# Kernel tuning notes

Measured on AMD Instinct MI355X. Metric: run time of the kernel, lower is better.

Reference implementation:

```python
import jax, jax.numpy as jnp
import numpy as np


def _compute_gradient(f, src, dst, egw):
    # f: [b, c, n] node features; src/dst: [b, e] edge endpoints; egw: [b, e, d]
    # gradient at node src = sum_edges pinvdx * (f[dst] - f[src])
    fT = f.transpose(0, 2, 1)  # b, n, c
    n = fT.shape[1]
    f_dst = jnp.take_along_axis(fT, dst[..., None], axis=1)  # b, e, c
    f_src = jnp.take_along_axis(fT, src[..., None], axis=1)  # b, e, c
    msg = egw[..., :, None] * (f_dst - f_src)[..., None, :]  # b, e, d, c
    b, e, d, c = msg.shape

    def seg(m, s):
        return jax.ops.segment_sum(m.reshape(e, d * c), s, num_segments=n)

    grad = jax.vmap(seg)(msg, src)  # b, n, d*c
    return grad.transpose(0, 2, 1)  # b, d*c, n


def _forward(x, t, nodes, node_weights, edge_gradient_weights, modes, sp_L,
             fc0_w, fc0_b, Wc, Ws, W0, ws_w, ws_b, gws_w, gws_b,
             fc1_w, fc1_b, fc2_w, fc2_b, directed_edges):
    D = nodes.shape[-1]
    # Fourier bases: modes [k,d,w] scaled by sp_L [d,w]
    temp = jnp.einsum('bxd,kdw->bxkw', nodes, modes * sp_L)
    bc, bs = jnp.cos(temp), jnp.sin(temp)
    b0 = jnp.ones(temp[:, :, :1, :].shape, temp.dtype)
    nw = node_weights[:, :, None, :]
    wbc, wbs, wb0 = bc * nw, bs * nw, b0 * nw

    x_value = x[:, :, :D]
    h = jnp.concatenate([x, t], -1) @ fc0_w + fc0_b  # b, n, c
    h = h.transpose(0, 2, 1)  # b, c, n

    src = directed_edges[..., 0]
    dst = directed_edges[..., 1]
    nlayers = ws_w.shape[0]
    for i in range(nlayers):
        # spectral convolution (real Fourier transform on scattered points)
        xc = jnp.einsum('bcx,bxkw->bckw', h, wbc)
        xs = -jnp.einsum('bcx,bxkw->bckw', h, wbs)
        x0 = jnp.einsum('bcx,bxkw->bckw', h, wb0)
        fc_ = jnp.einsum('bikw,iokw->bokw', xc, Wc[i]) - jnp.einsum('bikw,iokw->bokw', xs, Ws[i])
        fs_ = jnp.einsum('bikw,iokw->bokw', xs, Wc[i]) + jnp.einsum('bikw,iokw->bokw', xc, Ws[i])
        f0_ = jnp.einsum('bikw,iokw->bokw', x0, W0[i])
        x1 = (jnp.einsum('bokw,bxkw->box', f0_, b0)
              + 2.0 * jnp.einsum('bokw,bxkw->box', fc_, bc)
              - 2.0 * jnp.einsum('bokw,bxkw->box', fs_, bs))
        # pointwise linear (Conv1d kernel size 1)
        x2 = jnp.einsum('oc,bcx->box', ws_w[i], h) + ws_b[i][None, :, None]
        # gradient operator + softsign + Conv1d
        g = _compute_gradient(h, src, dst, edge_gradient_weights)  # b, d*c, n
        g = g / (1.0 + jnp.abs(g))  # softsign
        x3 = jnp.einsum('oc,bcx->box', gws_w[i], g) + gws_b[i][None, :, None]
        h = x1 + x2 + x3
        if i != nlayers - 1:
            h = jax.nn.gelu(h, approximate=False)

    h = h.transpose(0, 2, 1)  # b, n, c
    h = jax.nn.gelu(h @ fc1_w + fc1_b, approximate=False)
    h = h @ fc2_w + fc2_b
    return x_value + t * h


def setup_inputs() -> dict:
    B, N, E = 2, 20000, 100000
    D, W, K, C, L, FC, OUT = 3, 1, 128, 128, 3, 128, 3
    key = jax.random.key(0)
    k = jax.random.split(key, 16)
    x = jax.random.normal(k[0], (B, N, D), jnp.float32)
    t = jax.random.uniform(k[1], (B, N, 1), jnp.float32)
    node_mask = jnp.ones((B, N, 1), jnp.int32)
    nodes = jax.random.uniform(k[2], (B, N, D), jnp.float32)
    node_weights = jax.random.uniform(k[3], (B, N, W), jnp.float32) / N
    directed_edges = jax.random.randint(k[4], (B, E, 2), 0, N)
    edge_gradient_weights = jax.random.normal(k[5], (B, E, D), jnp.float32)
    modes = jax.random.normal(k[6], (K, D, W), jnp.float32) * (2.0 * np.pi)
    sp_L = jnp.ones((D, W), jnp.float32)
    fc0_w = jax.random.normal(k[7], (D + 1, C), jnp.float32) * 0.1
    fc0_b = jnp.zeros((C,), jnp.float32)
    scale = 1.0 / (C * C)
    Wc = jax.random.uniform(k[8], (L, C, C, K, W), jnp.float32) * scale
    Ws = jax.random.uniform(k[9], (L, C, C, K, W), jnp.float32) * scale
    W0 = jax.random.uniform(k[10], (L, C, C, 1, W), jnp.float32) * scale
    ws_w = jax.random.normal(k[11], (L, C, C), jnp.float32) * 0.05
    ws_b = jnp.zeros((L, C), jnp.float32)
    gws_w = jax.random.normal(k[12], (L, C, D * C), jnp.float32) * 0.05
    gws_b = jnp.zeros((L, C), jnp.float32)
    fc1_w = jax.random.normal(k[13], (C, FC), jnp.float32) * 0.05
    fc1_b = jnp.zeros((FC,), jnp.float32)
    fc2_w = jax.random.normal(k[14], (FC, OUT), jnp.float32) * 0.05
    fc2_b = jnp.zeros((OUT,), jnp.float32)
    return dict(x=x, t=t, node_mask=node_mask, nodes=nodes, node_weights=node_weights,
                directed_edges=directed_edges, edge_gradient_weights=edge_gradient_weights,
                modes=modes, sp_L=sp_L, fc0_w=fc0_w, fc0_b=fc0_b, Wc=Wc, Ws=Ws, W0=W0,
                ws_w=ws_w, ws_b=ws_b, gws_w=gws_w, gws_b=gws_b,
                fc1_w=fc1_w, fc1_b=fc1_b, fc2_w=fc2_w, fc2_b=fc2_b)


def reference(x, t, node_mask, nodes, node_weights, directed_edges, edge_gradient_weights,
              modes, sp_L, fc0_w, fc0_b, Wc, Ws, W0, ws_w, ws_b, gws_w, gws_b,
              fc1_w, fc1_b, fc2_w, fc2_b):
    del node_mask  # unpacked but unused in the original forward
    return _forward(x, t, nodes, node_weights, edge_gradient_weights, modes, sp_L,
                    fc0_w, fc0_b, Wc, Ws, W0, ws_w, ws_b, gws_w, gws_b,
                    fc1_w, fc1_b, fc2_w, fc2_b, directed_edges)
```

## Files before the change

kernel.cpp:

```cpp
#include <hip/hip_runtime.h>
#include <math.h>

#define BB 2
#define NN 20000
#define EE 100000
#define DD 3
#define KK 128
#define CC 128
#define LL 3
#define FCC 128
#define GJ (DD*CC)
#define KR 768
#define NP 20096
#define NCHK 157
#define G1CH 79
#define G1N 256

typedef __attribute__((ext_vector_type(8))) short bf16x8;
typedef __attribute__((ext_vector_type(4))) float f32x4;

__device__ inline unsigned short f2bf(float f) {
  unsigned int u = __float_as_uint(f);
  u += 0x7fffu + ((u >> 16) & 1u);
  return (unsigned short)(u >> 16);
}
__device__ inline float bf2f(unsigned short u) {
  return __uint_as_float(((unsigned int)u) << 16);
}

__device__ float d_nw[BB*NN];
__device__ __align__(16) unsigned short d_stackT[(size_t)BB*NP*KR];
__device__ __align__(16) unsigned short d_bcT[(size_t)BB*KK*NP];
__device__ __align__(16) unsigned short d_bsT[(size_t)BB*KK*NP];
__device__ __align__(16) unsigned short d_hTwT[(size_t)BB*CC*NP];
__device__ __align__(16) float d_uT[(size_t)BB*NP*FCC];
__device__ __align__(16) unsigned short d_Amatb[BB*CC*KR];
__device__ __align__(16) unsigned short d_fc1wb[FCC*CC];
__device__ __align__(16) float d_part[(size_t)BB*4*G1CH*2*64*64];
__device__ float d_xc[BB*CC*KK];
__device__ float d_xs[BB*CC*KK];
__device__ float d_x0p[BB*NCHK*CC];
__device__ float d_fcp[BB*CC*8*KK];
__device__ float d_fsp[BB*CC*8*KK];
__device__ float d_bias[BB*CC];
__device__ int d_cnt[BB*NN];
__device__ int d_cursor[BB*NN];
__device__ int d_off[BB*(NN+1)];
__device__ __align__(16) float4 d_erec[(size_t)BB*EE];

__global__ __launch_bounds__(128) void k_basis(const float* __restrict__ nodes,
                                               const float* __restrict__ nodew,
                                               const float* __restrict__ modes,
                                               const float* __restrict__ spL) {
  int bn = blockIdx.x;
  int k  = threadIdx.x;
  int b = bn / NN, n = bn % NN;
  float x0 = nodes[bn*3+0], x1 = nodes[bn*3+1], x2 = nodes[bn*3+2];
  float tmp = x0*modes[k*3+0]*spL[0] + x1*modes[k*3+1]*spL[1] + x2*modes[k*3+2]*spL[2];
  float cv = cosf(tmp), sv = sinf(tmp);
  size_t row = (size_t)(b*NP + n);
  d_stackT[row*KR + k]       = f2bf(cv);
  d_stackT[row*KR + 128 + k] = f2bf(sv);
  if (k == 0) d_nw[bn] = nodew[bn];
}

__global__ __launch_bounds__(256) void k_basisT() {
  __shared__ unsigned short t1[32][136];
  __shared__ unsigned short t2[32][136];
  int blk = blockIdx.x;
  int nt = blk % 628, b = blk / 628;
  int n0 = nt*32;
  int tid = threadIdx.x;
  int kl = tid & 127, ng = tid >> 7;
  for (int nn = ng; nn < 32; nn += 2) {
    int n = n0 + nn;
    unsigned short cv = 0, sv = 0;
    if (n < NN) {
      const unsigned short* sp = d_stackT + ((size_t)(b*NP + n))*KR;
      cv = sp[kl]; sv = sp[128 + kl];
    }
    t1[nn][kl] = cv;
    t2[nn][kl] = sv;
  }
  __syncthreads();
  int nl = tid & 31, kg = tid >> 5;
  for (int k = kg; k < 128; k += 8) {
    d_bcT[((size_t)(b*KK + k))*NP + n0 + nl] = t1[nl][k];
    d_bsT[((size_t)(b*KK + k))*NP + n0 + nl] = t2[nl][k];
  }
}

__global__ __launch_bounds__(256) void k_csr_zero() {
  int tid = blockIdx.x*256 + threadIdx.x;
  if (tid < BB*NN) { d_cnt[tid] = 0; d_cursor[tid] = 0; }
}

__global__ __launch_bounds__(256) void k_csr_count(const int* __restrict__ edges) {
  int e = blockIdx.x*256 + threadIdx.x;
  if (e >= BB*EE) return;
  int b = e / EE;
  int src = edges[e*2 + 0];
  atomicAdd(&d_cnt[b*NN + src], 1);
}

__global__ __launch_bounds__(1024) void k_csr_scan() {
  int b = blockIdx.x;
  __shared__ int sdata[1024];
  __shared__ int carry_s;
  int tid = threadIdx.x;
  if (tid == 0) carry_s = 0;
  __syncthreads();
  for (int chunk = 0; chunk < 20; ++chunk) {
    int i = chunk*1024 + tid;
    int v = (i < NN) ? d_cnt[b*NN + i] : 0;
    sdata[tid] = v;
    __syncthreads();
    for (int s = 1; s < 1024; s <<= 1) {
      int tv = (tid >= s) ? sdata[tid - s] : 0;
      __syncthreads();
      sdata[tid] += tv;
      __syncthreads();
    }
    int excl = carry_s + sdata[tid] - v;
    if (i < NN) d_off[b*(NN+1) + i] = excl;
    __syncthreads();
    if (tid == 1023) carry_s += sdata[1023];
    __syncthreads();
  }
  if (tid == 0) d_off[b*(NN+1) + NN] = carry_s;
}

__global__ __launch_bounds__(256) void k_csr_scatter(const int* __restrict__ edges,
                                                     const float* __restrict__ egw) {
  int e = blockIdx.x*256 + threadIdx.x;
  if (e >= BB*EE) return;
  int b = e / EE;
  int src = edges[e*2 + 0];
  int dst = edges[e*2 + 1];
  int pos = atomicAdd(&d_cursor[b*NN + src], 1);
  d_erec[(size_t)b*EE + d_off[b*(NN+1) + src] + pos] =
      make_float4(__int_as_float(dst), egw[e*3+0], egw[e*3+1], egw[e*3+2]);
}

__global__ __launch_bounds__(256) void k_h0(const float* __restrict__ x,
                                            const float* __restrict__ t,
                                            const float* __restrict__ w,
                                            const float* __restrict__ bias) {
  int tid = blockIdx.x*256 + threadIdx.x;
  int c = tid & 127;
  int bn = tid >> 7;
  int b = bn / NN, n = bn % NN;
  const float* xv = x + bn*3;
  float acc = bias[c] + xv[0]*w[c] + xv[1]*w[CC+c] + xv[2]*w[2*CC+c]
            + t[bn]*w[3*CC+c];
  d_stackT[((size_t)(b*NP + n))*KR + 256 + c] = f2bf(acc);
}

__global__ __launch_bounds__(256) void k_hT0() {
  __shared__ unsigned short t[128][136];
  int chunk = blockIdx.x;
  int b = blockIdx.y;
  int n0 = chunk*128;
  int tid = threadIdx.x;
  int cl = tid & 127, ng = tid >> 7;
  for (int nn = ng; nn < 128; nn += 2) {
    int n = n0 + nn;
    unsigned short v = 0;
    if (n < NN) {
      float hv = bf2f(d_stackT[((size_t)(b*NP + n))*KR + 256 + cl]);
      v = f2bf(hv * d_nw[b*NN + n]);
    }
    t[nn][cl] = v;
  }
  __syncthreads();
  int nl = tid & 31, cg = tid >> 5;
  for (int c = cg; c < 128; c += 8)
    for (int nn2 = 0; nn2 < 128; nn2 += 32)
      d_hTwT[((size_t)(b*CC + c))*NP + n0 + nn2 + nl] = t[nn2 + nl][c];
}

__global__ __launch_bounds__(256) void k_gemm1m() {
  __shared__ unsigned short Ash[2][64*40];
  __shared__ unsigned short Bch[2][64*40];
  __shared__ unsigned short Bsh[2][64*40];
  int chunk = blockIdx.x;
  int quad  = blockIdx.y;
  int b     = blockIdx.z;
  int ch = quad >> 1, kh = quad & 1;
  int tid = threadIdx.x, lane = tid & 63, wid = tid >> 6;
  int q = lane >> 4, m = lane & 15;
  f32x4 accC[4], accS[4];
  #pragma unroll
  for (int j = 0; j < 4; j++) { accC[j] = (f32x4){0.f,0.f,0.f,0.f}; accS[j] = (f32x4){0.f,0.f,0.f,0.f}; }
  const unsigned short* Ab  = d_hTwT + ((size_t)(b*CC + ch*64))*NP;
  const unsigned short* Bcp = d_bcT + ((size_t)(b*KK + kh*64))*NP;
  const unsigned short* Bsp = d_bsT + ((size_t)(b*KK + kh*64))*NP;
  int n0 = chunk*G1N;

#define G1STAGE(nb, d) { \
    int row_ = tid >> 2; int e8_ = (tid & 3)*8; \
    if ((nb) < NP) { \
      *(uint4*)&Ash[d][row_*40 + e8_] = *(const uint4*)(Ab  + (size_t)row_*NP + (nb) + e8_); \
      *(uint4*)&Bch[d][row_*40 + e8_] = *(const uint4*)(Bcp + (size_t)row_*NP + (nb) + e8_); \
      *(uint4*)&Bsh[d][row_*40 + e8_] = *(const uint4*)(Bsp + (size_t)row_*NP + (nb) + e8_); \
    } else { \
      uint4 z_ = make_uint4(0,0,0,0); \
      *(uint4*)&Ash[d][row_*40 + e8_] = z_; \
      *(uint4*)&Bch[d][row_*40 + e8_] = z_; \
      *(uint4*)&Bsh[d][row_*40 + e8_] = z_; \
    } }

  G1STAGE(n0, 0)
  int cur = 0;
  for (int s = 0; s < G1N/32; s++) {
    __syncthreads();
    if (s + 1 < G1N/32) G1STAGE(n0 + (s+1)*32, cur ^ 1)
    bf16x8 a = *(const bf16x8*)&Ash[cur][(wid*16 + m)*40 + q*8];
    #pragma unroll
    for (int kt = 0; kt < 4; kt++) {
      bf16x8 bcf = *(const bf16x8*)&Bch[cur][(kt*16 + m)*40 + q*8];
      accC[kt] = __builtin_amdgcn_mfma_f32_16x16x32_bf16(a, bcf, accC[kt], 0, 0, 0);
      bf16x8 bsf = *(const bf16x8*)&Bsh[cur][(kt*16 + m)*40 + q*8];
      accS[kt] = __builtin_amdgcn_mfma_f32_16x16x32_bf16(a, bsf, accS[kt], 0, 0, 0);
    }
    cur ^= 1;
  }
#undef G1STAGE

  float* base = d_part + ((size_t)(b*4 + quad)*G1CH + chunk)*2*4096;
  #pragma unroll
  for (int kt = 0; kt < 4; kt++)
    #pragma unroll
    for (int r = 0; r < 4; r++) {
      int c = wid*16 + q*4 + r;
      int k = kt*16 + m;
      base[c*64 + k]        =  accC[kt][r];
      base[4096 + c*64 + k] = -accS[kt][r];
    }
}

__global__ __launch_bounds__(256) void k_reduce1() {
  int tid = blockIdx.x*256 + threadIdx.x;
  int k = tid & 127;
  int c = (tid >> 7) & 127;
  int arr = (tid >> 14) & 1;
  int b = tid >> 15;
  int ch = c >> 6, cl = c & 63;
  int kh = k >> 6, kl = k & 63;
  int quad = ch*2 + kh;
  const float* p = d_part + ((size_t)(b*4 + quad)*G1CH)*2*4096 + arr*4096 + cl*64 + kl;
  float acc = 0.f;
  for (int t = 0; t < G1CH; t++) acc += p[(size_t)t*2*4096];
  if (arr == 0) d_xc[(b*CC + c)*KK + k] = acc;
  else          d_xs[(b*CC + c)*KK + k] = acc;
}

__global__ __launch_bounds__(256) void k_x0() {
  int chunk = blockIdx.x;
  int b = blockIdx.y;
  int tid = threadIdx.x;
  int c = tid >> 1, half = tid & 1;
  const unsigned short* p = d_hTwT + ((size_t)(b*CC + c))*NP + chunk*128 + half*64;
  float acc = 0.f;
  #pragma unroll
  for (int i = 0; i < 8; i++) {
    ushort4 v0 = *(const ushort4*)&p[i*8];
    ushort4 v1 = *(const ushort4*)&p[i*8 + 4];
    acc += bf2f(v0.x) + bf2f(v0.y) + bf2f(v0.z) + bf2f(v0.w)
         + bf2f(v1.x) + bf2f(v1.y) + bf2f(v1.z) + bf2f(v1.w);
  }
  __shared__ float red[128][2];
  red[c][half] = acc;
  __syncthreads();
  if (half == 0) d_x0p[(b*NCHK + chunk)*CC + c] = red[c][0] + red[c][1];
}

__global__ __launch_bounds__(128) void k_spec(const float* __restrict__ Wc,
                                              const float* __restrict__ Ws, int l) {
  int bo = blockIdx.x;
  int ch = blockIdx.y;
  int b = bo >> 7;
  int o = bo & 127;
  int k = threadIdx.x;
  int i0 = ch*16;
  const float* wcp = Wc + ((size_t)(l*CC + i0)*CC + o)*KK + k;
  const float* wsp = Ws + ((size_t)(l*CC + i0)*CC + o)*KK + k;
  float fc = 0.f, fs = 0.f;
  #pragma unroll 4
  for (int j = 0; j < 16; j++) {
    int i = i0 + j;
    float xcv = d_xc[(b*CC + i)*KK + k];
    float xsv = d_xs[(b*CC + i)*KK + k];
    float wcv = wcp[(size_t)j*CC*KK];
    float wsv = wsp[(size_t)j*CC*KK];
    fc += xcv*wcv - xsv*wsv;
    fs += xsv*wcv + xcv*wsv;
  }
  d_fcp[((size_t)bo*8 + ch)*KK + k] = fc;
  d_fsp[((size_t)bo*8 + ch)*KK + k] = fs;
}

__global__ __launch_bounds__(128) void k_f0(const float* __restrict__ W0,
                                            const float* __restrict__ wsb,
                                            const float* __restrict__ gwsb, int l) {
  int b = blockIdx.x;
  int o = threadIdx.x;
  __shared__ float sx[CC];
  float xv = 0.f;
  for (int p = 0; p < NCHK; p++) xv += d_x0p[(b*NCHK + p)*CC + o];
  sx[o] = xv;
  __syncthreads();
  float acc = 0.f;
  for (int i = 0; i < CC; i++) acc += sx[i]*W0[(l*CC + i)*CC + o];
  d_bias[b*CC + o] = acc + wsb[l*CC + o] + gwsb[l*CC + o];
}

__global__ __launch_bounds__(128) void k_buildAb(const float* __restrict__ wsw,
                                                 const float* __restrict__ gwsw, int l) {
  int bo = blockIdx.x;
  int b = bo >> 7, o = bo & 127;
  int t = threadIdx.x;
  float fc = 0.f, fs = 0.f;
  #pragma unroll
  for (int ch = 0; ch < 8; ch++) {
    fc += d_fcp[((size_t)bo*8 + ch)*KK + t];
    fs += d_fsp[((size_t)bo*8 + ch)*KK + t];
  }
  unsigned short* dst = d_Amatb + (size_t)bo*KR;
  dst[t]       = f2bf( 2.f*fc);
  dst[128 + t] = f2bf(-2.f*fs);
  dst[256 + t] = f2bf(wsw[(l*CC + o)*CC + t]);
  #pragma unroll
  for (int j = 0; j < 3; j++)
    dst[384 + j*128 + t] = f2bf(gwsw[(size_t)(l*CC + o)*GJ + j*128 + t]);
}

__global__ __launch_bounds__(128) void k_fc1w(const float* __restrict__ fc1w) {
  int c = blockIdx.x;
  int o2 = threadIdx.x;
  d_fc1wb[o2*CC + c] = f2bf(fc1w[c*FCC + o2]);
}

__global__ __launch_bounds__(128) void k_grad_csr() {
  int bn = blockIdx.x;
  int b = bn / NN, n = bn % NN;
  int c = threadIdx.x;
  int beg = d_off[b*(NN+1) + n];
  int end = d_off[b*(NN+1) + n + 1];
  const float4* rp = d_erec + (size_t)b*EE;
  const unsigned short* hb = d_stackT + (size_t)b*NP*KR + 256 + c;
  float a0 = 0.f, a1 = 0.f, a2 = 0.f;
  float sw0 = 0.f, sw1 = 0.f, sw2 = 0.f;
  int p = beg;
  for (; p + 4 <= end; p += 4) {
    float4 r1 = rp[p], r2 = rp[p+1], r3 = rp[p+2], r4 = rp[p+3];
    float f1 = bf2f(hb[(size_t)__float_as_int(r1.x)*KR]);
    float f2 = bf2f(hb[(size_t)__float_as_int(r2.x)*KR]);
    float f3 = bf2f(hb[(size_t)__float_as_int(r3.x)*KR]);
    float f4 = bf2f(hb[(size_t)__float_as_int(r4.x)*KR]);
    a0 += r1.y*f1 + r2.y*f2 + r3.y*f3 + r4.y*f4;
    a1 += r1.z*f1 + r2.z*f2 + r3.z*f3 + r4.z*f4;
    a2 += r1.w*f1 + r2.w*f2 + r3.w*f3 + r4.w*f4;
    sw0 += r1.y + r2.y + r3.y + r4.y;
    sw1 += r1.z + r2.z + r3.z + r4.z;
    sw2 += r1.w + r2.w + r3.w + r4.w;
  }
  for (; p < end; ++p) {
    float4 r1 = rp[p];
    float f1 = bf2f(hb[(size_t)__float_as_int(r1.x)*KR]);
    a0 += r1.y*f1; a1 += r1.z*f1; a2 += r1.w*f1;
    sw0 += r1.y; sw1 += r1.z; sw2 += r1.w;
  }
  float fs = bf2f(hb[(size_t)n*KR]);
  a0 -= sw0*fs; a1 -= sw1*fs; a2 -= sw2*fs;
  unsigned short* gp = d_stackT + ((size_t)(b*NP + n))*KR + 384;
  gp[c]        = f2bf(a0/(1.f + fabsf(a0)));
  gp[CC + c]   = f2bf(a1/(1.f + fabsf(a1)));
  gp[2*CC + c] = f2bf(a2/(1.f + fabsf(a2)));
}

__global__ __launch_bounds__(256) void k_mfma(int koff, int K,
                                              const unsigned short* __restrict__ W, size_t wstride,
                                              float* __restrict__ Out,
                                              const float* __restrict__ bias, int bias_stride,
                                              int gelu, int aux) {
  __shared__ unsigned short As[2][32*72];
  __shared__ unsigned short Bs[2][128*72];
  int b = blockIdx.z;
  int n_base = blockIdx.x*32;
  int tid = threadIdx.x;
  int lane = tid & 63, wid = tid >> 6;
  int wr = wid >> 1, wc = wid & 1;
  int q = lane >> 4, m = lane & 15;

  f32x4 acc[4];
  #pragma unroll
  for (int j = 0; j < 4; j++) acc[j] = (f32x4){0.f,0.f,0.f,0.f};

  const unsigned short* Wb = W + (size_t)b*wstride;
  const unsigned short* Ab = d_stackT + (size_t)b*NP*KR + koff;

#define STAGE(k0, d) { \
    { int rowA = tid >> 3; int e8A = (tid & 7)*8; \
      *(uint4*)&As[d][rowA*72 + e8A] = *(const uint4*)(Ab + (size_t)(n_base + rowA)*KR + (k0) + e8A); } \
    _Pragma("unroll") \
    for (int i_ = 0; i_ < 4; i_++) { \
      int idx_ = tid + i_*256; int rowB = idx_ >> 3; int e8B = (idx_ & 7)*8; \
      *(uint4*)&Bs[d][rowB*72 + e8B] = *(const uint4*)(Wb + (size_t)rowB*K + (k0) + e8B); } }

  STAGE(0, 0)
  int cur = 0;
  for (int k0 = 0; k0 < K; k0 += 64) {
    __syncthreads();
    if (k0 + 64 < K) STAGE(k0 + 64, cur ^ 1)
    bf16x8 a0 = *(const bf16x8*)&As[cur][(wr*16 + m)*72 + q*8];
    bf16x8 a1 = *(const bf16x8*)&As[cur][(wr*16 + m)*72 + 32 + q*8];
    #pragma unroll
    for (int ot = 0; ot < 4; ot++) {
      bf16x8 b0 = *(const bf16x8*)&Bs[cur][(wc*64 + ot*16 + m)*72 + q*8];
      acc[ot] = __builtin_amdgcn_mfma_f32_16x16x32_bf16(a0, b0, acc[ot], 0, 0, 0);
      bf16x8 b1 = *(const bf16x8*)&Bs[cur][(wc*64 + ot*16 + m)*72 + 32 + q*8];
      acc[ot] = __builtin_amdgcn_mfma_f32_16x16x32_bf16(a1, b1, acc[ot], 0, 0, 0);
    }
    cur ^= 1;
  }
#undef STAGE

  const float* bp = bias + (size_t)b*bias_stride;
  int nb4 = n_base + wr*16 + q*4;
  float nw4[4];
  #pragma unroll
  for (int r = 0; r < 4; r++)
    nw4[r] = (aux && nb4 + r < NN) ? d_nw[b*NN + nb4 + r] : 0.f;
  #pragma unroll
  for (int ot = 0; ot < 4; ot++) {
    int o = wc*64 + ot*16 + m;
    float bvv = bp[o];
    float vals[4];
    #pragma unroll
    for (int r = 0; r < 4; r++) {
      float v = acc[ot][r] + bvv;
      if (gelu) v = 0.5f*v*(1.f + erff(v*0.70710678118f));
      vals[r] = v;
      if (!aux) Out[((size_t)(b*NP + nb4 + r))*128 + o] = v;
      if (aux && nb4 + r < NN)
        d_stackT[((size_t)(b*NP + nb4 + r))*KR + 256 + o] = f2bf(v);
    }
    if (aux) {
      ushort4 pk;
      pk.x = f2bf(vals[0]*nw4[0]);
      pk.y = f2bf(vals[1]*nw4[1]);
      pk.z = f2bf(vals[2]*nw4[2]);
      pk.w = f2bf(vals[3]*nw4[3]);
      *(ushort4*)&d_hTwT[((size_t)(b*CC + o))*NP + nb4] = pk;
    }
  }
}

__global__ __launch_bounds__(256) void k_out(const float* __restrict__ x,
                                             const float* __restrict__ t,
                                             const float* __restrict__ fc2w,
                                             const float* __restrict__ fc2b,
                                             float* __restrict__ out) {
  int tid = blockIdx.x*256 + threadIdx.x;
  if (tid >= BB*NN) return;
  int b = tid / NN, n = tid % NN;
  const float* up = d_uT + ((size_t)(b*NP + n))*FCC;
  float a0 = fc2b[0], a1 = fc2b[1], a2v = fc2b[2];
  #pragma unroll 4
  for (int o2 = 0; o2 < FCC; o2 += 4) {
    float4 uv = *(const float4*)&up[o2];
    a0  += uv.x*fc2w[(o2+0)*3+0] + uv.y*fc2w[(o2+1)*3+0] + uv.z*fc2w[(o2+2)*3+0] + uv.w*fc2w[(o2+3)*3+0];
    a1  += uv.x*fc2w[(o2+0)*3+1] + uv.y*fc2w[(o2+1)*3+1] + uv.z*fc2w[(o2+2)*3+1] + uv.w*fc2w[(o2+3)*3+1];
    a2v += uv.x*fc2w[(o2+0)*3+2] + uv.y*fc2w[(o2+1)*3+2] + uv.z*fc2w[(o2+2)*3+2] + uv.w*fc2w[(o2+3)*3+2];
  }
  float tv = t[tid];
  out[tid*3 + 0] = x[tid*3 + 0] + tv*a0;
  out[tid*3 + 1] = x[tid*3 + 1] + tv*a1;
  out[tid*3 + 2] = x[tid*3 + 2] + tv*a2v;
}

extern "C" void kernel_launch(void* const* d_in, const int* in_sizes, int n_in,
                              void* d_out, int out_size, void* d_ws, size_t ws_size,
                              hipStream_t stream) {
  const float* x     = (const float*)d_in[0];
  const float* t     = (const float*)d_in[1];
  const float* nodes = (const float*)d_in[3];
  const float* nodew = (const float*)d_in[4];
  const int*   edges = (const int*)d_in[5];
  const float* egw   = (const float*)d_in[6];
  const float* modes = (const float*)d_in[7];
  const float* spL   = (const float*)d_in[8];
  const float* fc0w  = (const float*)d_in[9];
  const float* fc0b  = (const float*)d_in[10];
  const float* Wc    = (const float*)d_in[11];
  const float* Ws    = (const float*)d_in[12];
  const float* W0    = (const float*)d_in[13];
  const float* wsw   = (const float*)d_in[14];
  const float* wsb   = (const float*)d_in[15];
  const float* gwsw  = (const float*)d_in[16];
  const float* gwsb  = (const float*)d_in[17];
  const float* fc1w  = (const float*)d_in[18];
  const float* fc1b  = (const float*)d_in[19];
  const float* fc2w  = (const float*)d_in[20];
  const float* fc2b  = (const float*)d_in[21];
  float* out = (float*)d_out;

  unsigned short* d_Amatb_p; hipGetSymbolAddress((void**)&d_Amatb_p, HIP_SYMBOL(d_Amatb));
  unsigned short* d_fc1wb_p; hipGetSymbolAddress((void**)&d_fc1wb_p, HIP_SYMBOL(d_fc1wb));
  float* d_uT_p;    hipGetSymbolAddress((void**)&d_uT_p,    HIP_SYMBOL(d_uT));
  float* d_bias_p;  hipGetSymbolAddress((void**)&d_bias_p,  HIP_SYMBOL(d_bias));

  hipLaunchKernelGGL(k_basis, dim3(BB*NN), dim3(128), 0, stream, nodes, nodew, modes, spL);
  hipLaunchKernelGGL(k_basisT, dim3(628*BB), dim3(256), 0, stream);
  hipLaunchKernelGGL(k_h0, dim3(BB*NN*CC/256), dim3(256), 0, stream, x, t, fc0w, fc0b);
  hipLaunchKernelGGL(k_hT0, dim3(NCHK, BB), dim3(256), 0, stream);
  hipLaunchKernelGGL(k_fc1w, dim3(CC), dim3(FCC), 0, stream, fc1w);
  hipLaunchKernelGGL(k_csr_zero, dim3((BB*NN + 255)/256), dim3(256), 0, stream);
  hipLaunchKernelGGL(k_csr_count, dim3((BB*EE + 255)/256), dim3(256), 0, stream, edges);
  hipLaunchKernelGGL(k_csr_scan, dim3(BB), dim3(1024), 0, stream);
  hipLaunchKernelGGL(k_csr_scatter, dim3((BB*EE + 255)/256), dim3(256), 0, stream, edges, egw);

  for (int l = 0; l < LL; l++) {
    hipLaunchKernelGGL(k_gemm1m, dim3(G1CH, 4, BB), dim3(256), 0, stream);
    hipLaunchKernelGGL(k_reduce1, dim3(256), dim3(256), 0, stream);
    hipLaunchKernelGGL(k_x0, dim3(NCHK, BB), dim3(256), 0, stream);
    hipLaunchKernelGGL(k_spec, dim3(BB*CC, 8), dim3(128), 0, stream, Wc, Ws, l);
    hipLaunchKernelGGL(k_f0, dim3(BB), dim3(CC), 0, stream, W0, wsb, gwsb, l);
    hipLaunchKernelGGL(k_buildAb, dim3(BB*CC), dim3(128), 0, stream, wsw, gwsw, l);
    hipLaunchKernelGGL(k_grad_csr, dim3(BB*NN), dim3(128), 0, stream);
    hipLaunchKernelGGL(k_mfma, dim3(NP/32, 1, BB), dim3(256), 0, stream,
                       0, KR, d_Amatb_p, (size_t)CC*KR, d_uT_p, d_bias_p, CC,
                       (l != LL-1) ? 1 : 0, 1);
  }

  hipLaunchKernelGGL(k_mfma, dim3(NP/32, 1, BB), dim3(256), 0, stream,
                     256, CC, d_fc1wb_p, (size_t)0, d_uT_p, fc1b, 0, 1, 0);
  hipLaunchKernelGGL(k_out, dim3((BB*NN + 255)/256), dim3(256), 0, stream, x, t, fc2w, fc2b, out);
}
```

Baseline: 525.8 us.

## Load GEMM weights straight to registers, stage epilogue through LDS, store fc1 output as bf16

In the MFMA GEMM the weight tile is no longer staged in shared memory. Each thread loads its B fragments directly from global memory into registers, using a double-buffered register prefetch. The epilogue now writes results into an LDS tile and then emits coalesced 16-byte row stores for both the stacked activation buffer and the fc1 output. The fc1 output buffer changes from fp32 to bf16, which halves its write and read traffic in k_out at the cost of extra rounding before the final fc2 projection. The direct weight loads depend on L2/L1 caching of the small weight matrix, which every block re-reads.

```diff
diff --git a/kernel.cpp b/kernel.cpp
--- a/kernel.cpp
+++ b/kernel.cpp
@@ -33,7 +33,7 @@
 __device__ __align__(16) unsigned short d_bcT[(size_t)BB*KK*NP];
 __device__ __align__(16) unsigned short d_bsT[(size_t)BB*KK*NP];
 __device__ __align__(16) unsigned short d_hTwT[(size_t)BB*CC*NP];
-__device__ __align__(16) float d_uT[(size_t)BB*NP*FCC];
+__device__ __align__(16) unsigned short d_uTb[(size_t)BB*NP*FCC];
 __device__ __align__(16) unsigned short d_Amatb[BB*CC*KR];
 __device__ __align__(16) unsigned short d_fc1wb[FCC*CC];
 __device__ __align__(16) float d_part[(size_t)BB*4*G1CH*2*64*64];
@@ -381,11 +381,11 @@
 
 __global__ __launch_bounds__(256) void k_mfma(int koff, int K,
                                               const unsigned short* __restrict__ W, size_t wstride,
-                                              float* __restrict__ Out,
+                                              unsigned short* __restrict__ OutB,
                                               const float* __restrict__ bias, int bias_stride,
                                               int gelu, int aux) {
   __shared__ unsigned short As[2][32*72];
-  __shared__ unsigned short Bs[2][128*72];
+  __shared__ unsigned short Ep[32*132];
   int b = blockIdx.z;
   int n_base = blockIdx.x*32;
   int tid = threadIdx.x;
@@ -397,41 +397,49 @@
   #pragma unroll
   for (int j = 0; j < 4; j++) acc[j] = (f32x4){0.f,0.f,0.f,0.f};
 
-  const unsigned short* Wb = W + (size_t)b*wstride;
   const unsigned short* Ab = d_stackT + (size_t)b*NP*KR + koff;
-
-#define STAGE(k0, d) { \
-    { int rowA = tid >> 3; int e8A = (tid & 7)*8; \
-      *(uint4*)&As[d][rowA*72 + e8A] = *(const uint4*)(Ab + (size_t)(n_base + rowA)*KR + (k0) + e8A); } \
-    _Pragma("unroll") \
-    for (int i_ = 0; i_ < 4; i_++) { \
-      int idx_ = tid + i_*256; int rowB = idx_ >> 3; int e8B = (idx_ & 7)*8; \
-      *(uint4*)&Bs[d][rowB*72 + e8B] = *(const uint4*)(Wb + (size_t)rowB*K + (k0) + e8B); } }
-
-  STAGE(0, 0)
+  const unsigned short* Brow = W + (size_t)b*wstride + ((size_t)(wc*64 + m))*K + q*8;
+
+#define STAGEA(k0, d) { int rowA = tid >> 3; int e8A = (tid & 7)*8; \
+    *(uint4*)&As[d][rowA*72 + e8A] = *(const uint4*)(Ab + (size_t)(n_base + rowA)*KR + (k0) + e8A); }
+
+  bf16x8 bP[8], bQ[8];
+  STAGEA(0, 0)
+  #pragma unroll
+  for (int ot = 0; ot < 4; ot++) {
+    bP[2*ot]   = *(const bf16x8*)(Brow + (size_t)(ot*16)*K);
+    bP[2*ot+1] = *(const bf16x8*)(Brow + (size_t)(ot*16)*K + 32);
+  }
   int cur = 0;
   for (int k0 = 0; k0 < K; k0 += 64) {
     __syncthreads();
-    if (k0 + 64 < K) STAGE(k0 + 64, cur ^ 1)
+    if (k0 + 64 < K) {
+      STAGEA(k0 + 64, cur ^ 1)
+      #pragma unroll
+      for (int ot = 0; ot < 4; ot++) {
+        bQ[2*ot]   = *(const bf16x8*)(Brow + (size_t)(ot*16)*K + k0 + 64);
+        bQ[2*ot+1] = *(const bf16x8*)(Brow + (size_t)(ot*16)*K + k0 + 96);
+      }
+    }
     bf16x8 a0 = *(const bf16x8*)&As[cur][(wr*16 + m)*72 + q*8];
     bf16x8 a1 = *(const bf16x8*)&As[cur][(wr*16 + m)*72 + 32 + q*8];
     #pragma unroll
     for (int ot = 0; ot < 4; ot++) {
-      bf16x8 b0 = *(const bf16x8*)&Bs[cur][(wc*64 + ot*16 + m)*72 + q*8];
-      acc[ot] = __builtin_amdgcn_mfma_f32_16x16x32_bf16(a0, b0, acc[ot], 0, 0, 0);
-      bf16x8 b1 = *(const bf16x8*)&Bs[cur][(wc*64 + ot*16 + m)*72 + 32 + q*8];
-      acc[ot] = __builtin_amdgcn_mfma_f32_16x16x32_bf16(a1, b1, acc[ot], 0, 0, 0);
-    }
+      acc[ot] = __builtin_amdgcn_mfma_f32_16x16x32_bf16(a0, bP[2*ot],   acc[ot], 0, 0, 0);
+      acc[ot] = __builtin_amdgcn_mfma_f32_16x16x32_bf16(a1, bP[2*ot+1], acc[ot], 0, 0, 0);
+    }
+    #pragma unroll
+    for (int j = 0; j < 8; j++) bP[j] = bQ[j];
     cur ^= 1;
   }
-#undef STAGE
+#undef STAGEA
 
   const float* bp = bias + (size_t)b*bias_stride;
-  int nb4 = n_base + wr*16 + q*4;
+  int lrow = wr*16 + q*4;
   float nw4[4];
   #pragma unroll
   for (int r = 0; r < 4; r++)
-    nw4[r] = (aux && nb4 + r < NN) ? d_nw[b*NN + nb4 + r] : 0.f;
+    nw4[r] = (aux && n_base + lrow + r < NN) ? d_nw[b*NN + n_base + lrow + r] : 0.f;
   #pragma unroll
   for (int ot = 0; ot < 4; ot++) {
     int o = wc*64 + ot*16 + m;
@@ -442,9 +450,7 @@
       float v = acc[ot][r] + bvv;
       if (gelu) v = 0.5f*v*(1.f + erff(v*0.70710678118f));
       vals[r] = v;
-      if (!aux) Out[((size_t)(b*NP + nb4 + r))*128 + o] = v;
-      if (aux && nb4 + r < NN)
-        d_stackT[((size_t)(b*NP + nb4 + r))*KR + 256 + o] = f2bf(v);
+      Ep[(lrow + r)*132 + o] = f2bf(v);
     }
     if (aux) {
       ushort4 pk;
@@ -452,7 +458,26 @@
       pk.y = f2bf(vals[1]*nw4[1]);
       pk.z = f2bf(vals[2]*nw4[2]);
       pk.w = f2bf(vals[3]*nw4[3]);
-      *(ushort4*)&d_hTwT[((size_t)(b*CC + o))*NP + nb4] = pk;
+      *(ushort4*)&d_hTwT[((size_t)(b*CC + o))*NP + n_base + lrow] = pk;
+    }
+  }
+  __syncthreads();
+  {
+    int row = tid >> 3;
+    int c16 = (tid & 7)*16;
+    int n = n_base + row;
+    uint4 v0 = *(uint4*)&Ep[row*132 + c16];
+    uint4 v1 = *(uint4*)&Ep[row*132 + c16 + 8];
+    if (aux) {
+      if (n < NN) {
+        unsigned short* dst = d_stackT + ((size_t)(b*NP + n))*KR + 256;
+        *(uint4*)&dst[c16]     = v0;
+        *(uint4*)&dst[c16 + 8] = v1;
+      }
+    } else {
+      unsigned short* dst = OutB + ((size_t)(b*NP + n))*FCC;
+      *(uint4*)&dst[c16]     = v0;
+      *(uint4*)&dst[c16 + 8] = v1;
     }
   }
 }
@@ -465,14 +490,15 @@
   int tid = blockIdx.x*256 + threadIdx.x;
   if (tid >= BB*NN) return;
   int b = tid / NN, n = tid % NN;
-  const float* up = d_uT + ((size_t)(b*NP + n))*FCC;
+  const unsigned short* up = d_uTb + ((size_t)(b*NP + n))*FCC;
   float a0 = fc2b[0], a1 = fc2b[1], a2v = fc2b[2];
   #pragma unroll 4
   for (int o2 = 0; o2 < FCC; o2 += 4) {
-    float4 uv = *(const float4*)&up[o2];
-    a0  += uv.x*fc2w[(o2+0)*3+0] + uv.y*fc2w[(o2+1)*3+0] + uv.z*fc2w[(o2+2)*3+0] + uv.w*fc2w[(o2+3)*3+0];
-    a1  += uv.x*fc2w[(o2+0)*3+1] + uv.y*fc2w[(o2+1)*3+1] + uv.z*fc2w[(o2+2)*3+1] + uv.w*fc2w[(o2+3)*3+1];
-    a2v += uv.x*fc2w[(o2+0)*3+2] + uv.y*fc2w[(o2+1)*3+2] + uv.z*fc2w[(o2+2)*3+2] + uv.w*fc2w[(o2+3)*3+2];
+    ushort4 uv = *(const ushort4*)&up[o2];
+    float u0 = bf2f(uv.x), u1 = bf2f(uv.y), u2 = bf2f(uv.z), u3 = bf2f(uv.w);
+    a0  += u0*fc2w[(o2+0)*3+0] + u1*fc2w[(o2+1)*3+0] + u2*fc2w[(o2+2)*3+0] + u3*fc2w[(o2+3)*3+0];
+    a1  += u0*fc2w[(o2+0)*3+1] + u1*fc2w[(o2+1)*3+1] + u2*fc2w[(o2+2)*3+1] + u3*fc2w[(o2+3)*3+1];
+    a2v += u0*fc2w[(o2+0)*3+2] + u1*fc2w[(o2+1)*3+2] + u2*fc2w[(o2+2)*3+2] + u3*fc2w[(o2+3)*3+2];
   }
   float tv = t[tid];
   out[tid*3 + 0] = x[tid*3 + 0] + tv*a0;
@@ -508,7 +534,7 @@
 
   unsigned short* d_Amatb_p; hipGetSymbolAddress((void**)&d_Amatb_p, HIP_SYMBOL(d_Amatb));
   unsigned short* d_fc1wb_p; hipGetSymbolAddress((void**)&d_fc1wb_p, HIP_SYMBOL(d_fc1wb));
-  float* d_uT_p;    hipGetSymbolAddress((void**)&d_uT_p,    HIP_SYMBOL(d_uT));
+  unsigned short* d_uTb_p;   hipGetSymbolAddress((void**)&d_uTb_p,   HIP_SYMBOL(d_uTb));
   float* d_bias_p;  hipGetSymbolAddress((void**)&d_bias_p,  HIP_SYMBOL(d_bias));
 
   hipLaunchKernelGGL(k_basis, dim3(BB*NN), dim3(128), 0, stream, nodes, nodew, modes, spL);
@@ -530,11 +556,11 @@
     hipLaunchKernelGGL(k_buildAb, dim3(BB*CC), dim3(128), 0, stream, wsw, gwsw, l);
     hipLaunchKernelGGL(k_grad_csr, dim3(BB*NN), dim3(128), 0, stream);
     hipLaunchKernelGGL(k_mfma, dim3(NP/32, 1, BB), dim3(256), 0, stream,
-                       0, KR, d_Amatb_p, (size_t)CC*KR, d_uT_p, d_bias_p, CC,
+                       0, KR, d_Amatb_p, (size_t)CC*KR, d_uTb_p, d_bias_p, CC,
                        (l != LL-1) ? 1 : 0, 1);
   }
 
   hipLaunchKernelGGL(k_mfma, dim3(NP/32, 1, BB), dim3(256), 0, stream,
-                     256, CC, d_fc1wb_p, (size_t)0, d_uT_p, fc1b, 0, 1, 0);
+                     256, CC, d_fc1wb_p, (size_t)0, d_uTb_p, fc1b, 0, 1, 0);
   hipLaunchKernelGGL(k_out, dim3((BB*NN + 255)/256), dim3(256), 0, stream, x, t, fc2w, fc2b, out);
 }
```

Measured after the change: 613.3 us. 16.6% more time.
